# Kernel tuning notes

Measured on AMD Instinct MI355X. Metric: run time of the kernel, lower is better.

The kernel has to match this reference:

```python
import jax, jax.numpy as jnp
import numpy as np

NUM_TRUE = 8
NUM_NULL = 2
NUM_EXPERTS = NUM_TRUE + NUM_NULL
TOP_K = 2


def setup_inputs() -> dict:
    key = jax.random.key(0)
    k0, k1, k2 = jax.random.split(key, 3)
    B, S, D = 4, 2048, 1024
    inputs = jax.random.normal(k0, (B, S, D), dtype=jnp.float32)
    gate_w = jax.random.normal(k1, (NUM_EXPERTS, D), dtype=jnp.float32) * 0.02
    gate_b = jnp.zeros((NUM_EXPERTS,), dtype=jnp.float32)
    # expert_w stored as [E, D_in, D_out] so expert i computes x @ expert_w[i] + expert_b[i]
    expert_w = jax.random.normal(k2, (NUM_TRUE, D, D), dtype=jnp.float32) * 0.02
    expert_b = jnp.zeros((NUM_TRUE, D), dtype=jnp.float32)
    return {"inputs": inputs, "gate_w": gate_w, "gate_b": gate_b,
            "expert_w": expert_w, "expert_b": expert_b}


def reference(inputs, gate_w, gate_b, expert_w, expert_b):
    D = inputs.shape[-1]
    x = inputs.reshape(-1, D)                       # [T, D]
    gate_logits = x @ gate_w.T + gate_b             # [T, E]
    gate_probs = jax.nn.softmax(gate_logits, axis=-1)
    weights, selected = jax.lax.top_k(gate_probs, TOP_K)  # [T, K]
    true_mask = selected < NUM_TRUE                 # null experts contribute nothing
    true_weights = weights * true_mask
    denom = true_weights.sum(axis=-1, keepdims=True)
    denom = jnp.where(denom > 0, denom, jnp.ones_like(denom))
    norm_w = (true_weights / denom).astype(x.dtype)  # [T, K]
    # per-(token, true-expert) combine weight; zero for unselected experts
    one_hot = jax.nn.one_hot(selected, NUM_EXPERTS, dtype=norm_w.dtype)  # [T, K, E]
    combine_w = jnp.einsum('tk,tke->te', norm_w, one_hot)[:, :NUM_TRUE]  # [T, E_true]
    # dense expert evaluation, then weighted combine (zero weights cancel
    # exactly as the gather/scatter loop in the torch code)
    expert_out = jnp.einsum('td,edh->teh', x, expert_w) + expert_b[None, :, :]  # [T, E_true, D]
    out = jnp.einsum('te,teh->th', combine_w, expert_out)  # [T, D]
    return out.reshape(inputs.shape[:-1] + (out.shape[-1],))
```

## Files before the change

### kernel.cpp

```cpp
#include <hip/hip_runtime.h>
#include <hip/hip_bf16.h>
#include <stdint.h>

#define T_TOKENS 8192
#define D_DIM    1024
#define NE       10
#define NT       8
#define SEG      2048

typedef unsigned short u16;
typedef __attribute__((ext_vector_type(8))) __bf16 bf16x8;
typedef __attribute__((ext_vector_type(4))) float  f32x4;
typedef __attribute__((ext_vector_type(8))) unsigned short u16x8;
typedef __attribute__((ext_vector_type(4))) unsigned short u16x4;

static __device__ __forceinline__ u16 f32_to_bf16(float f) {
  union { float f; uint32_t u; } v; v.f = f;
  uint32_t u = v.u;
  return (u16)((u + 0x7fffu + ((u >> 16) & 1u)) >> 16);
}
static __device__ __forceinline__ float bf16_to_f32(u16 u) {
  union { uint32_t u; float f; } v; v.u = ((uint32_t)u) << 16; return v.f;
}

static __device__ __forceinline__ void async_load16(const u16* g, u16* l) {
  __builtin_amdgcn_global_load_lds(
      (const __attribute__((address_space(1))) void*)(const void*)g,
      (__attribute__((address_space(3))) void*)(void*)l, 16, 0, 0);
}

union PrepShared {
  struct { float gws[NE * D_DIM]; float gbs[NE]; int se[32]; float swt[32]; } g;
  struct { float tile[64][65]; } t;
};

__global__ __launch_bounds__(256) void prep_kernel(
    const float* __restrict__ x, const float* __restrict__ gw,
    const float* __restrict__ gb, const float* __restrict__ W,
    u16* __restrict__ xb, u16* __restrict__ wT,
    int* __restrict__ cnt, int* __restrict__ tokList,
    int* __restrict__ revIdx, float* __restrict__ revW) {
  __shared__ PrepShared sh;
  int tid = threadIdx.x;

  if (blockIdx.x >= 512) {
    int tb = blockIdx.x - 512;
    int e  = tb >> 8;
    int rem = tb & 255;
    int k0 = (rem >> 4) * 64;
    int n0 = (rem & 15) * 64;
    int c  = tid & 63;
    int r0 = tid >> 6;
    const float* We = W + ((size_t)e << 20);
#pragma unroll
    for (int rr = 0; rr < 16; ++rr) {
      int r = rr * 4 + r0;
      sh.t.tile[c][r] = We[(size_t)(k0 + r) * 1024 + n0 + c];
    }
    __syncthreads();
    u16* wTe = wT + ((size_t)e << 20);
#pragma unroll
    for (int rr = 0; rr < 16; ++rr) {
      int n = rr * 4 + r0;
      wTe[(size_t)(n0 + n) * 1024 + k0 + c] = f32_to_bf16(sh.t.tile[n][c]);
    }
    return;
  }

  {
    const f32x4* g4 = (const f32x4*)gw;
    f32x4* s4 = (f32x4*)sh.g.gws;
    for (int i = tid; i < NE * D_DIM / 4; i += 256) s4[i] = g4[i];
  }
  if (tid < NE) sh.g.gbs[tid] = gb[tid];
  __syncthreads();
  int lane = tid & 63;
  int wv   = tid >> 6;
  const f32x4* gws4 = (const f32x4*)sh.g.gws;
  for (int it = 0; it < 4; ++it) {
    int slot = wv * 4 + it;
    int t = blockIdx.x * 16 + slot;
    const f32x4* xr4 = (const f32x4*)(x + (size_t)t * D_DIM);
    f32x4 xv[4];
#pragma unroll
    for (int jj = 0; jj < 4; ++jj) xv[jj] = xr4[lane + 64 * jj];
    u16x4* xbr = (u16x4*)(xb + (size_t)t * D_DIM);
#pragma unroll
    for (int jj = 0; jj < 4; ++jj) {
      u16x4 pk;
#pragma unroll
      for (int k = 0; k < 4; ++k) pk[k] = f32_to_bf16(xv[jj][k]);
      xbr[lane + 64 * jj] = pk;
    }
    float logit[NE];
#pragma unroll
    for (int e = 0; e < NE; ++e) {
      float a = 0.f;
#pragma unroll
      for (int jj = 0; jj < 4; ++jj) {
        f32x4 gv = gws4[e * 256 + lane + 64 * jj];
#pragma unroll
        for (int k = 0; k < 4; ++k) a = fmaf(xv[jj][k], gv[k], a);
      }
#pragma unroll
      for (int off = 32; off >= 1; off >>= 1) a += __shfl_xor(a, off);
      logit[e] = a + sh.g.gbs[e];
    }
    float mx = logit[0];
#pragma unroll
    for (int e = 1; e < NE; ++e) mx = fmaxf(mx, logit[e]);
    float p[NE]; float s = 0.f;
#pragma unroll
    for (int e = 0; e < NE; ++e) { p[e] = expf(logit[e] - mx); s += p[e]; }
    int e0 = 0; float b0 = p[0];
#pragma unroll
    for (int e = 1; e < NE; ++e) if (p[e] > b0) { b0 = p[e]; e0 = e; }
    int e1 = -1; float b1 = -1.f;
#pragma unroll
    for (int e = 0; e < NE; ++e) if (e != e0 && p[e] > b1) { b1 = p[e]; e1 = e; }
    float w0 = b0 / s, w1 = b1 / s;
    float tw0 = (e0 < NT) ? w0 : 0.f;
    float tw1 = (e1 < NT) ? w1 : 0.f;
    float denom = tw0 + tw1;
    float nw0 = 0.f, nw1 = 0.f;
    if (denom > 0.f) { nw0 = tw0 / denom; nw1 = tw1 / denom; }
    if (lane == 0) {
      sh.g.se[slot * 2]     = (e0 < NT) ? e0 : -1;  sh.g.swt[slot * 2]     = nw0;
      sh.g.se[slot * 2 + 1] = (e1 < NT) ? e1 : -1;  sh.g.swt[slot * 2 + 1] = nw1;
      if (e0 >= NT) { revIdx[t * 2]     = -1; revW[t * 2]     = 0.f; }
      if (e1 >= NT) { revIdx[t * 2 + 1] = -1; revW[t * 2 + 1] = 0.f; }
    }
  }
  __syncthreads();
  if (tid < NT) {
    int e = tid, c = 0;
    for (int i = 0; i < 32; ++i) c += (sh.g.se[i] == e);
    if (c > 0) {
      int base = atomicAdd(&cnt[e * 32], c);
      int j = 0;
      for (int i = 0; i < 32; ++i) {
        if (sh.g.se[i] == e) {
          int tt  = blockIdx.x * 16 + (i >> 1);
          int pos = base + j;
          tokList[e * SEG + pos]   = tt;
          revIdx[tt * 2 + (i & 1)] = e * SEG + pos;
          revW[tt * 2 + (i & 1)]   = sh.g.swt[i];
          ++j;
        }
      }
    }
  }
}

__global__ __launch_bounds__(256) void moe_gemm(
    const u16* __restrict__ xb, const u16* __restrict__ wT,
    const int* __restrict__ cnt, const int* __restrict__ tokList,
    const float* __restrict__ eb, u16* __restrict__ ybuf) {
  int e  = blockIdx.x;
  int c  = cnt[e * 32];
  int m0 = blockIdx.z * 128;
  if (m0 >= c) return;
  int n0 = blockIdx.y * 128;
  __shared__ __align__(16) u16 As[3][128 * 32];
  __shared__ __align__(16) u16 Bs[3][128 * 32];
  __shared__ int tokS[128];
  int tid = threadIdx.x;
  if (tid < 128) {
    int gm = m0 + tid;
    tokS[tid] = (gm < c) ? tokList[e * SEG + gm] : tokList[e * SEG];
  }
  __syncthreads();
  int lane = tid & 63;
  int wv   = tid >> 6;
  int rl  = lane >> 2;
  int kcp = lane & 3;
  int kcd = kcp ^ (rl & 3);
  int rowL0 = wv * 32 + rl, rowL1 = rowL0 + 16;
  const u16* gA0 = xb + (size_t)tokS[rowL0] * 1024 + kcd * 8;
  const u16* gA1 = xb + (size_t)tokS[rowL1] * 1024 + kcd * 8;
  const u16* wTe = wT + ((size_t)e << 20);
  const u16* gB0 = wTe + (size_t)(n0 + rowL0) * 1024 + kcd * 8;
  const u16* gB1 = wTe + (size_t)(n0 + rowL1) * 1024 + kcd * 8;
  int ldsA0 = (wv * 32) * 32, ldsA1 = (wv * 32 + 16) * 32;

  int wm = wv >> 1, wn = wv & 1;
  int lrow = lane & 15;
  int q    = lane >> 4;
  int sw   = (q ^ (lrow & 3)) * 8;
  f32x4 acc[4][4];
#pragma unroll
  for (int i = 0; i < 4; ++i)
#pragma unroll
    for (int j = 0; j < 4; ++j) acc[i][j] = (f32x4){0.f, 0.f, 0.f, 0.f};

#pragma unroll
  for (int p = 0; p < 2; ++p) {
    int ko = p * 32;
    async_load16(gA0 + ko, As[p] + ldsA0);
    async_load16(gA1 + ko, As[p] + ldsA1);
    async_load16(gB0 + ko, Bs[p] + ldsA0);
    async_load16(gB1 + ko, Bs[p] + ldsA1);
  }

  int cur = 0;
  for (int kt = 0; kt < 32; ++kt) {
    asm volatile("s_barrier" ::: "memory");
    if (kt < 30) {
      int st = cur - 1; if (st < 0) st += 3;
      int ko = (kt + 2) * 32;
      async_load16(gA0 + ko, As[st] + ldsA0);
      async_load16(gA1 + ko, As[st] + ldsA1);
      async_load16(gB0 + ko, Bs[st] + ldsA0);
      async_load16(gB1 + ko, Bs[st] + ldsA1);
      asm volatile("s_waitcnt vmcnt(8)" ::: "memory");
    } else if (kt == 30) {
      asm volatile("s_waitcnt vmcnt(4)" ::: "memory");
    } else {
      asm volatile("s_waitcnt vmcnt(0)" ::: "memory");
    }
    asm volatile("s_barrier" ::: "memory");
    bf16x8 af[4], bfr[4];
#pragma unroll
    for (int mt = 0; mt < 4; ++mt)
      af[mt] = *(const bf16x8*)(As[cur] + (wm * 64 + mt * 16 + lrow) * 32 + sw);
#pragma unroll
    for (int nt = 0; nt < 4; ++nt)
      bfr[nt] = *(const bf16x8*)(Bs[cur] + (wn * 64 + nt * 16 + lrow) * 32 + sw);
#pragma unroll
    for (int mt = 0; mt < 4; ++mt)
#pragma unroll
      for (int nt = 0; nt < 4; ++nt)
        acc[mt][nt] = __builtin_amdgcn_mfma_f32_16x16x32_bf16(
            af[mt], bfr[nt], acc[mt][nt], 0, 0, 0);
    ++cur; if (cur == 3) cur = 0;
  }
  int rq = lane >> 4;
  float bias[4];
#pragma unroll
  for (int nt = 0; nt < 4; ++nt)
    bias[nt] = eb[e * 1024 + n0 + wn * 64 + nt * 16 + lrow];
  u16* yb = ybuf + ((size_t)(e * SEG + m0)) * 1024 + n0 + wn * 64 + lrow;
#pragma unroll
  for (int mt = 0; mt < 4; ++mt) {
#pragma unroll
    for (int r = 0; r < 4; ++r) {
      int ml = wm * 64 + mt * 16 + rq * 4 + r;
      u16* row = yb + (size_t)ml * 1024;
#pragma unroll
      for (int nt = 0; nt < 4; ++nt)
        row[nt * 16] = f32_to_bf16(acc[mt][nt][r] + bias[nt]);
    }
  }
}

__global__ __launch_bounds__(256) void combine_kernel(
    const u16* __restrict__ ybuf, const int* __restrict__ revIdx,
    const float* __restrict__ revW, float* __restrict__ out) {
  int tid = threadIdx.x, lane = tid & 63, wv = tid >> 6;
  for (int it = 0; it < 4; ++it) {
    int t  = blockIdx.x * 16 + wv * 4 + it;
    int i0 = revIdx[t * 2], i1 = revIdx[t * 2 + 1];
    float w0 = revW[t * 2], w1 = revW[t * 2 + 1];
    float o[16];
#pragma unroll
    for (int k = 0; k < 16; ++k) o[k] = 0.f;
    if (i0 >= 0) {
      const u16x8* y = (const u16x8*)(ybuf + (size_t)i0 * 1024);
#pragma unroll
      for (int jj = 0; jj < 2; ++jj) {
        u16x8 v = y[lane + 64 * jj];
#pragma unroll
        for (int k = 0; k < 8; ++k) o[jj * 8 + k] += w0 * bf16_to_f32(v[k]);
      }
    }
    if (i1 >= 0) {
      const u16x8* y = (const u16x8*)(ybuf + (size_t)i1 * 1024);
#pragma unroll
      for (int jj = 0; jj < 2; ++jj) {
        u16x8 v = y[lane + 64 * jj];
#pragma unroll
        for (int k = 0; k < 8; ++k) o[jj * 8 + k] += w1 * bf16_to_f32(v[k]);
      }
    }
    f32x4* o4 = (f32x4*)(out + (size_t)t * 1024);
#pragma unroll
    for (int jj = 0; jj < 2; ++jj)
#pragma unroll
      for (int h = 0; h < 2; ++h) {
        f32x4 vv = {o[jj * 8 + h * 4], o[jj * 8 + h * 4 + 1],
                    o[jj * 8 + h * 4 + 2], o[jj * 8 + h * 4 + 3]};
        o4[2 * (lane + 64 * jj) + h] = vv;
      }
  }
}

extern "C" void kernel_launch(void* const* d_in, const int* in_sizes, int n_in,
                              void* d_out, int out_size, void* d_ws, size_t ws_size,
                              hipStream_t stream) {
  const float* x  = (const float*)d_in[0];
  const float* gw = (const float*)d_in[1];
  const float* gb = (const float*)d_in[2];
  const float* ew = (const float*)d_in[3];
  const float* eb = (const float*)d_in[4];
  float* out = (float*)d_out;
  char* ws = (char*)d_ws;
  int*   cnt     = (int*)ws;
  int*   tokList = (int*)(ws + 4096);
  int*   revIdx  = (int*)(ws + 4096 + 65536);
  float* revW    = (float*)(ws + 4096 + 131072);
  u16*   xb      = (u16*)(ws + 200704);
  u16*   wT      = (u16*)(ws + 200704 + 16777216);
  u16*   ybuf    = (u16*)(ws + 200704 + 33554432);

  hipMemsetAsync(cnt, 0, 4096, stream);
  prep_kernel<<<2560, 256, 0, stream>>>(x, gw, gb, ew, xb, wT, cnt, tokList,
                                        revIdx, revW);
  moe_gemm<<<dim3(8, 8, 16), 256, 0, stream>>>(xb, wT, cnt, tokList, eb, ybuf);
  combine_kernel<<<512, 256, 0, stream>>>(ybuf, revIdx, revW, out);
}
```

Measured before the change: 178.5 us.

## Use 512-thread GEMM blocks, vectorize weight transpose, nontemporal output stores

The expert GEMM now runs 8 waves per 128x128 tile, each wave computing a 64x32 sub-tile, and each thread issues one A and one B async load per stage. The LDS swizzle and the waitcnt values are adjusted to match. The weight transpose/convert now reads float4 and writes packed 4xbf16, with a padded LDS tile. The combine kernel writes its output with nontemporal stores. The aim is more latency hiding in the GEMM and fewer memory instructions in prep, at the cost of less per-wave register reuse and possible LDS bank conflicts from the new tile[68] stride.

After: 181.4 us. About the same (+1.6%).

```diff
diff --git a/kernel.cpp b/kernel.cpp
--- a/kernel.cpp
+++ b/kernel.cpp
@@ -31,7 +31,7 @@
 
 union PrepShared {
   struct { float gws[NE * D_DIM]; float gbs[NE]; int se[32]; float swt[32]; } g;
-  struct { float tile[64][65]; } t;
+  struct { float tile[64][68]; } t;
 };
 
 __global__ __launch_bounds__(256) void prep_kernel(
@@ -49,20 +49,26 @@
     int rem = tb & 255;
     int k0 = (rem >> 4) * 64;
     int n0 = (rem & 15) * 64;
-    int c  = tid & 63;
-    int r0 = tid >> 6;
+    int cr = tid & 15;
+    int r0 = tid >> 4;
     const float* We = W + ((size_t)e << 20);
 #pragma unroll
-    for (int rr = 0; rr < 16; ++rr) {
-      int r = rr * 4 + r0;
-      sh.t.tile[c][r] = We[(size_t)(k0 + r) * 1024 + n0 + c];
+    for (int pass = 0; pass < 4; ++pass) {
+      int r = pass * 16 + r0;
+      f32x4 v = *(const f32x4*)&We[(size_t)(k0 + r) * 1024 + n0 + cr * 4];
+#pragma unroll
+      for (int j = 0; j < 4; ++j) sh.t.tile[cr * 4 + j][r] = v[j];
     }
     __syncthreads();
     u16* wTe = wT + ((size_t)e << 20);
 #pragma unroll
-    for (int rr = 0; rr < 16; ++rr) {
-      int n = rr * 4 + r0;
-      wTe[(size_t)(n0 + n) * 1024 + k0 + c] = f32_to_bf16(sh.t.tile[n][c]);
+    for (int pass = 0; pass < 4; ++pass) {
+      int n = pass * 16 + r0;
+      f32x4 tv = *(const f32x4*)&sh.t.tile[n][cr * 4];
+      u16x4 pk;
+#pragma unroll
+      for (int j = 0; j < 4; ++j) pk[j] = f32_to_bf16(tv[j]);
+      *(u16x4*)&wTe[(size_t)(n0 + n) * 1024 + k0 + cr * 4] = pk;
     }
     return;
   }
@@ -152,7 +158,7 @@
   }
 }
 
-__global__ __launch_bounds__(256) void moe_gemm(
+__global__ __launch_bounds__(512) void moe_gemm(
     const u16* __restrict__ xb, const u16* __restrict__ wT,
     const int* __restrict__ cnt, const int* __restrict__ tokList,
     const float* __restrict__ eb, u16* __restrict__ ybuf) {
@@ -174,32 +180,28 @@
   int wv   = tid >> 6;
   int rl  = lane >> 2;
   int kcp = lane & 3;
-  int kcd = kcp ^ (rl & 3);
-  int rowL0 = wv * 32 + rl, rowL1 = rowL0 + 16;
-  const u16* gA0 = xb + (size_t)tokS[rowL0] * 1024 + kcd * 8;
-  const u16* gA1 = xb + (size_t)tokS[rowL1] * 1024 + kcd * 8;
+  int kcd = kcp ^ ((rl >> 1) & 3);
+  int rowL = wv * 16 + rl;
+  const u16* gA0 = xb + (size_t)tokS[rowL] * 1024 + kcd * 8;
   const u16* wTe = wT + ((size_t)e << 20);
-  const u16* gB0 = wTe + (size_t)(n0 + rowL0) * 1024 + kcd * 8;
-  const u16* gB1 = wTe + (size_t)(n0 + rowL1) * 1024 + kcd * 8;
-  int ldsA0 = (wv * 32) * 32, ldsA1 = (wv * 32 + 16) * 32;
-
-  int wm = wv >> 1, wn = wv & 1;
+  const u16* gB0 = wTe + (size_t)(n0 + rowL) * 1024 + kcd * 8;
+  int ldsO = (wv * 16) * 32;
+
+  int wm = wv >> 2, wn = wv & 3;
   int lrow = lane & 15;
   int q    = lane >> 4;
-  int sw   = (q ^ (lrow & 3)) * 8;
-  f32x4 acc[4][4];
+  int sw   = (q ^ ((lrow >> 1) & 3)) * 8;
+  f32x4 acc[4][2];
 #pragma unroll
   for (int i = 0; i < 4; ++i)
 #pragma unroll
-    for (int j = 0; j < 4; ++j) acc[i][j] = (f32x4){0.f, 0.f, 0.f, 0.f};
+    for (int j = 0; j < 2; ++j) acc[i][j] = (f32x4){0.f, 0.f, 0.f, 0.f};
 
 #pragma unroll
   for (int p = 0; p < 2; ++p) {
     int ko = p * 32;
-    async_load16(gA0 + ko, As[p] + ldsA0);
-    async_load16(gA1 + ko, As[p] + ldsA1);
-    async_load16(gB0 + ko, Bs[p] + ldsA0);
-    async_load16(gB1 + ko, Bs[p] + ldsA1);
+    async_load16(gA0 + ko, As[p] + ldsO);
+    async_load16(gB0 + ko, Bs[p] + ldsO);
   }
 
   int cur = 0;
@@ -208,38 +210,36 @@
     if (kt < 30) {
       int st = cur - 1; if (st < 0) st += 3;
       int ko = (kt + 2) * 32;
-      async_load16(gA0 + ko, As[st] + ldsA0);
-      async_load16(gA1 + ko, As[st] + ldsA1);
-      async_load16(gB0 + ko, Bs[st] + ldsA0);
-      async_load16(gB1 + ko, Bs[st] + ldsA1);
-      asm volatile("s_waitcnt vmcnt(8)" ::: "memory");
+      async_load16(gA0 + ko, As[st] + ldsO);
+      async_load16(gB0 + ko, Bs[st] + ldsO);
+      asm volatile("s_waitcnt vmcnt(4)" ::: "memory");
     } else if (kt == 30) {
-      asm volatile("s_waitcnt vmcnt(4)" ::: "memory");
+      asm volatile("s_waitcnt vmcnt(2)" ::: "memory");
     } else {
       asm volatile("s_waitcnt vmcnt(0)" ::: "memory");
     }
     asm volatile("s_barrier" ::: "memory");
-    bf16x8 af[4], bfr[4];
+    bf16x8 af[4], bfr[2];
 #pragma unroll
     for (int mt = 0; mt < 4; ++mt)
       af[mt] = *(const bf16x8*)(As[cur] + (wm * 64 + mt * 16 + lrow) * 32 + sw);
 #pragma unroll
-    for (int nt = 0; nt < 4; ++nt)
-      bfr[nt] = *(const bf16x8*)(Bs[cur] + (wn * 64 + nt * 16 + lrow) * 32 + sw);
+    for (int nt = 0; nt < 2; ++nt)
+      bfr[nt] = *(const bf16x8*)(Bs[cur] + (wn * 32 + nt * 16 + lrow) * 32 + sw);
 #pragma unroll
     for (int mt = 0; mt < 4; ++mt)
 #pragma unroll
-      for (int nt = 0; nt < 4; ++nt)
+      for (int nt = 0; nt < 2; ++nt)
         acc[mt][nt] = __builtin_amdgcn_mfma_f32_16x16x32_bf16(
             af[mt], bfr[nt], acc[mt][nt], 0, 0, 0);
     ++cur; if (cur == 3) cur = 0;
   }
   int rq = lane >> 4;
-  float bias[4];
-#pragma unroll
-  for (int nt = 0; nt < 4; ++nt)
-    bias[nt] = eb[e * 1024 + n0 + wn * 64 + nt * 16 + lrow];
-  u16* yb = ybuf + ((size_t)(e * SEG + m0)) * 1024 + n0 + wn * 64 + lrow;
+  float bias[2];
+#pragma unroll
+  for (int nt = 0; nt < 2; ++nt)
+    bias[nt] = eb[e * 1024 + n0 + wn * 32 + nt * 16 + lrow];
+  u16* yb = ybuf + ((size_t)(e * SEG + m0)) * 1024 + n0 + wn * 32 + lrow;
 #pragma unroll
   for (int mt = 0; mt < 4; ++mt) {
 #pragma unroll
@@ -247,7 +247,7 @@
       int ml = wm * 64 + mt * 16 + rq * 4 + r;
       u16* row = yb + (size_t)ml * 1024;
 #pragma unroll
-      for (int nt = 0; nt < 4; ++nt)
+      for (int nt = 0; nt < 2; ++nt)
         row[nt * 16] = f32_to_bf16(acc[mt][nt][r] + bias[nt]);
     }
   }
@@ -289,7 +289,7 @@
       for (int h = 0; h < 2; ++h) {
         f32x4 vv = {o[jj * 8 + h * 4], o[jj * 8 + h * 4 + 1],
                     o[jj * 8 + h * 4 + 2], o[jj * 8 + h * 4 + 3]};
-        o4[2 * (lane + 64 * jj) + h] = vv;
+        __builtin_nontemporal_store(vv, &o4[2 * (lane + 64 * jj) + h]);
       }
   }
 }
@@ -315,6 +315,6 @@
   hipMemsetAsync(cnt, 0, 4096, stream);
   prep_kernel<<<2560, 256, 0, stream>>>(x, gw, gb, ew, xb, wT, cnt, tokList,
                                         revIdx, revW);
-  moe_gemm<<<dim3(8, 8, 16), 256, 0, stream>>>(xb, wT, cnt, tokList, eb, ybuf);
+  moe_gemm<<<dim3(8, 8, 16), 512, 0, stream>>>(xb, wT, cnt, tokList, eb, ybuf);
   combine_kernel<<<512, 256, 0, stream>>>(ybuf, revIdx, revW, out);
 }
```
